# Kernel optimization log

Measured on AMD Instinct MI355X. Metric: run time of the kernel, lower is better.

## Reference

```python
import jax, jax.numpy as jnp
import numpy as np

H = 2048          # hidden_size
I = 1408          # moe_intermediate_size
E = 32            # n_routed_experts
K = 4             # num_experts_per_tok
NS = 2            # n_shared_experts
RG = RU = RD = 128  # CUR ranks
SI = I * NS       # shared-expert intermediate size
B, S = 2, 2048


def _init(key, shape, fan_in):
    return jax.random.normal(key, shape, jnp.float32) / np.sqrt(fan_in)


def setup_inputs() -> dict:
    ks = jax.random.split(jax.random.key(0), 20)
    return {
        'x': jax.random.normal(ks[0], (B, S, H), jnp.float32),
        'gate_w': _init(ks[1], (E, H), H),
        'Rg': _init(ks[2], (RG, H), H),
        'Ru': _init(ks[3], (RU, H), H),
        'Rd': _init(ks[4], (RD, I), I),
        'Ug': _init(ks[5], (E, RG, RG), RG),
        'Cg': _init(ks[6], (E, I, RG), RG),
        'Uu': _init(ks[7], (E, RU, RU), RU),
        'Cu': _init(ks[8], (E, I, RU), RU),
        'Ud': _init(ks[9], (E, RD, RD), RD),
        'Cd': _init(ks[10], (E, H, RD), RD),
        's_Rg': _init(ks[11], (RG, H), H),
        's_Ug': _init(ks[12], (RG, RG), RG),
        's_Cg': _init(ks[13], (SI, RG), RG),
        's_Ru': _init(ks[14], (RU, H), H),
        's_Uu': _init(ks[15], (RU, RU), RU),
        's_Cu': _init(ks[16], (SI, RU), RU),
        's_Rd': _init(ks[17], (RD, SI), SI),
        's_Ud': _init(ks[18], (RD, RD), RD),
        's_Cd': _init(ks[19], (H, RD), RD),
    }


def _moe_forward(x, gate_w, Rg, Ru, Rd, Ug, Cg, Uu, Cu, Ud, Cd,
                 s_Rg, s_Ug, s_Cg, s_Ru, s_Uu, s_Cu, s_Rd, s_Ud, s_Cd):
    Bv, Sv, Hv = x.shape
    xf = x.reshape(-1, Hv)                       # [T,H]
    T = xf.shape[0]

    # ---- top-k softmax gate ----
    logits = xf @ gate_w.T                       # [T,E]
    scores = jax.nn.softmax(logits, axis=-1)
    tw, ti = jax.lax.top_k(scores, K)            # [T,K]
    tw = tw / (tw.sum(-1, keepdims=True) + 1e-20)
    # dense per-(token,expert) combine weight; zero where token not routed.
    # Mathematically identical to the torch gather/per-expert-GEMM/scatter_add path.
    we = jnp.zeros((T, E), xf.dtype).at[jnp.arange(T)[:, None], ti].add(tw)  # [T,E]

    # shared R projections are expert-independent: compute once for all tokens
    rg = xf @ Rg.T                               # [T,RG]
    ru = xf @ Ru.T                               # [T,RU]

    def expert_fn(Ug_e, Cg_e, Uu_e, Cu_e, Ud_e, Cd_e, w_e, rg, ru):
        g = jax.nn.silu((rg @ Ug_e.T) @ Cg_e.T)  # [T,I]
        u = (ru @ Uu_e.T) @ Cu_e.T               # [T,I]
        rd = (g * u) @ Rd.T                      # [T,RD]
        return w_e[:, None] * ((rd @ Ud_e.T) @ Cd_e.T)  # [T,H]

    expert_fn = jax.checkpoint(expert_fn)

    def body(acc, ws):
        Ug_e, Cg_e, Uu_e, Cu_e, Ud_e, Cd_e, w_e = ws
        return acc + expert_fn(Ug_e, Cg_e, Uu_e, Cu_e, Ud_e, Cd_e, w_e, rg, ru), None

    y, _ = jax.lax.scan(body, jnp.zeros_like(xf), (Ug, Cg, Uu, Cu, Ud, Cd, we.T))

    # ---- shared experts (own R matrices, intermediate = I * n_shared) ----
    g = jax.nn.silu(((xf @ s_Rg.T) @ s_Ug.T) @ s_Cg.T)   # [T,SI]
    u = ((xf @ s_Ru.T) @ s_Uu.T) @ s_Cu.T                # [T,SI]
    sh = (((g * u) @ s_Rd.T) @ s_Ud.T) @ s_Cd.T          # [T,H]

    return (y + sh).reshape(Bv, Sv, Hv)


def reference(x, gate_w, Rg, Ru, Rd, Ug, Cg, Uu, Cu, Ud, Cd,
              s_Rg, s_Ug, s_Cg, s_Ru, s_Uu, s_Cu, s_Rd, s_Ud, s_Cd):
    return _moe_forward(x, gate_w, Rg, Ru, Rd, Ug, Cg, Uu, Cu, Ud, Cd,
                        s_Rg, s_Ug, s_Cg, s_Ru, s_Uu, s_Cu, s_Rd, s_Ud, s_Cd)
```

## Files before the change

kernel.cpp:

```cpp
#include <hip/hip_runtime.h>
#include <math.h>

#define T_TOK 4096
#define HD    2048
#define NEXP  32
#define IR    1408
#define ISH   2816
#define NPAIR (T_TOK*4)
#define SRK   136
#define MTILES 11

typedef unsigned short ushort_t;
typedef __attribute__((ext_vector_type(8))) short    short8;
typedef __attribute__((ext_vector_type(8))) __bf16   bf16x8;
typedef __attribute__((ext_vector_type(4))) float    f32x4;

__device__ __forceinline__ f32x4 MF(short8 a, short8 b, f32x4 c) {
  return __builtin_amdgcn_mfma_f32_16x16x32_bf16(
      __builtin_bit_cast(bf16x8, a), __builtin_bit_cast(bf16x8, b), c, 0, 0, 0);
}
__device__ __forceinline__ ushort_t f2b(float f) {
  unsigned u = __float_as_uint(f);
  unsigned r = (u + 0x7fffu + ((u >> 16) & 1u)) >> 16;
  return (ushort_t)r;
}
__device__ __forceinline__ float b2f(ushort_t b) {
  return __uint_as_float(((unsigned)b) << 16);
}

__device__ __forceinline__ void gll16(const ushort_t* g, ushort_t* l) {
  __builtin_amdgcn_global_load_lds(
      (const __attribute__((address_space(1))) unsigned int*)(const void*)g,
      (__attribute__((address_space(3))) unsigned int*)(void*)l, 16, 0, 0);
}

__device__ __forceinline__ void load_64x128_swz(
    const ushort_t* __restrict__ g, size_t gstride, ushort_t* lds, int tid)
{
  const int lane = tid & 63, w = tid >> 6;
  #pragma unroll
  for (int s = 0; s < 4; ++s) {
    int rbase = s*16 + w*4;
    int r = rbase + (lane >> 4);
    int p = lane & 15;
    gll16(g + (size_t)r*gstride + ((p ^ (r & 15)) << 3), lds + rbase*128);
  }
}

#define NSEG 19
struct CvtSegs {
  const float* s[NSEG];
  ushort_t* d[NSEG];
  int n4[NSEG];
  int blk0[NSEG+1];
};
__global__ __launch_bounds__(256) void cvt_all_kernel(CvtSegs cs)
{
  int b = blockIdx.x;
  int k = 0;
  #pragma unroll 1
  while (k+1 < NSEG && b >= cs.blk0[k+1]) ++k;
  int i = (b - cs.blk0[k])*256 + threadIdx.x;
  if (i < cs.n4[k]) {
    float4 v = ((const float4*)cs.s[k])[i];
    ushort4 o; o.x=f2b(v.x); o.y=f2b(v.y); o.z=f2b(v.z); o.w=f2b(v.w);
    ((ushort4*)cs.d[k])[i] = o;
  }
}

__global__ __launch_bounds__(256) void gate_kernel(
    const float* __restrict__ x, const float* __restrict__ gw,
    int* __restrict__ topk_idx, float* __restrict__ topk_w, int* __restrict__ cnt)
{
  __shared__ float gws[32*132];
  __shared__ float xs[4*132];
  const int tid = threadIdx.x;
  const int w = tid >> 6, lane = tid & 63;
  const int t0 = blockIdx.x * 4;
  const int e = lane & 31, half = lane >> 5;

  float acc = 0.f;
  for (int ck = 0; ck < HD/128; ++ck) {
    for (int li = tid; li < 1024; li += 256) {
      int r = li >> 5, c4 = li & 31;
      *(float4*)(gws + r*132 + c4*4) = *(const float4*)(gw + (size_t)r*HD + ck*128 + c4*4);
    }
    for (int li = tid; li < 128; li += 256) {
      int r = li >> 5, c4 = li & 31;
      *(float4*)(xs + r*132 + c4*4) = *(const float4*)(x + (size_t)(t0+r)*HD + ck*128 + c4*4);
    }
    __syncthreads();
    #pragma unroll
    for (int k4 = 0; k4 < 16; ++k4) {
      float4 xv = *(const float4*)(xs + w*132 + half*64 + k4*4);
      float4 wv = *(const float4*)(gws + e*132 + half*64 + k4*4);
      acc += xv.x*wv.x + xv.y*wv.y + xv.z*wv.z + xv.w*wv.w;
    }
    __syncthreads();
  }
  float p = acc;
  p += __shfl_down(p, 32);
  float logit = (lane < 32) ? p : -INFINITY;
  float m = logit;
  #pragma unroll
  for (int o = 32; o >= 1; o >>= 1) m = fmaxf(m, __shfl_xor(m, o));
  float ex = (lane < 32) ? expf(logit - m) : 0.f;
  float se = ex;
  #pragma unroll
  for (int o = 32; o >= 1; o >>= 1) se += __shfl_xor(se, o);
  float score = ex / se;

  bool taken = false;
  float selw[4]; int seli[4];
  for (int k = 0; k < 4; ++k) {
    float cur = (lane < 32 && !taken) ? score : -1.f;
    float mm = cur;
    #pragma unroll
    for (int o = 32; o >= 1; o >>= 1) mm = fmaxf(mm, __shfl_xor(mm, o));
    unsigned long long b = __ballot(cur == mm);
    int il = __ffsll(b) - 1;
    if (lane == il) taken = true;
    selw[k] = mm; seli[k] = il;
  }
  float wsum = selw[0]+selw[1]+selw[2]+selw[3] + 1e-20f;
  int t = t0 + w;
  if (lane < 4) {
    topk_idx[t*4+lane] = seli[lane];
    topk_w[t*4+lane]  = selw[lane] / wsum;
    atomicAdd(&cnt[seli[lane]], 1);
  }
}

__global__ void scan_kernel(const int* __restrict__ cnt, int* __restrict__ offA)
{
  if (threadIdx.x == 0) {
    int a = 0;
    for (int e = 0; e < NEXP; ++e) { offA[e] = a; a += cnt[e]; }
    offA[NEXP] = a;
  }
}

__global__ __launch_bounds__(256) void scatter_kernel(
    const int* __restrict__ topk_idx, const float* __restrict__ topk_w,
    const int* __restrict__ offA, int* __restrict__ fill,
    int* __restrict__ list_tok, int* __restrict__ slot_of)
{
  int t = blockIdx.x*256 + threadIdx.x;
  if (t >= T_TOK) return;
  #pragma unroll
  for (int k = 0; k < 4; ++k) {
    int e = topk_idx[t*4+k];
    int pos = atomicAdd(&fill[e], 1);
    int s = offA[e] + pos;
    list_tok[s] = t;
    slot_of[t*4+k] = s;
  }
}

__global__ __launch_bounds__(256) void rproj_kernel(
    const ushort_t* __restrict__ xb,
    const ushort_t* __restrict__ Rg, const ushort_t* __restrict__ Ru,
    const ushort_t* __restrict__ sRg, const ushort_t* __restrict__ sRu,
    ushort_t* __restrict__ rg, ushort_t* __restrict__ ru,
    ushort_t* __restrict__ sa, ushort_t* __restrict__ su)
{
  __shared__ ushort_t abuf[2][64*128];
  const ushort_t* W; ushort_t* Y;
  switch (blockIdx.y) {
    case 0:  W = Rg;  Y = rg; break;
    case 1:  W = Ru;  Y = ru; break;
    case 2:  W = sRg; Y = sa; break;
    default: W = sRu; Y = su; break;
  }
  const int tid = threadIdx.x;
  const int lane = tid & 63, ln = lane & 15, q = lane >> 4;
  const int wv = tid >> 6, mh = wv >> 1, nh = wv & 1;
  const int r0 = blockIdx.x * 64;

  f32x4 acc[2][4];
  #pragma unroll
  for (int i = 0; i < 2; ++i)
    #pragma unroll
    for (int j = 0; j < 4; ++j) acc[i][j] = (f32x4){0.f,0.f,0.f,0.f};

  load_64x128_swz(xb + (size_t)r0*HD, HD, abuf[0], tid);
  for (int kt = 0; kt < 16; ++kt) {
    __syncthreads();
    if (kt+1 < 16)
      load_64x128_swz(xb + (size_t)r0*HD + (kt+1)*128, HD, abuf[(kt+1)&1], tid);
    const ushort_t* A = abuf[kt&1];
    #pragma unroll
    for (int c = 0; c < 4; ++c) {
      short8 a[2], b[4];
      #pragma unroll
      for (int i = 0; i < 2; ++i) {
        int rr = mh*32 + i*16 + ln;
        a[i] = *(const short8*)(A + rr*128 + (((c*4+q) ^ (rr&15)) << 3));
      }
      #pragma unroll
      for (int j = 0; j < 4; ++j)
        b[j] = *(const short8*)(W + (size_t)(nh*64 + j*16 + ln)*HD + kt*128 + c*32 + q*8);
      #pragma unroll
      for (int i = 0; i < 2; ++i)
        #pragma unroll
        for (int j = 0; j < 4; ++j) acc[i][j] = MF(a[i], b[j], acc[i][j]);
    }
  }
  #pragma unroll
  for (int i = 0; i < 2; ++i)
    #pragma unroll
    for (int j = 0; j < 4; ++j)
      #pragma unroll
      for (int r = 0; r < 4; ++r)
        Y[(size_t)(r0 + mh*32 + i*16 + q*4 + r)*128 + nh*64 + j*16 + ln] = f2b(acc[i][j][r]);
}

__device__ __forceinline__ void gemm64x128_regs(
    int tid, const ushort_t* __restrict__ A, const ushort_t* __restrict__ Wg,
    ushort_t* __restrict__ stage, f32x4 acc[2][2][2])
{
  const int lane = tid & 63, ln = lane & 15, q = lane >> 4;
  const int wv = tid >> 6, mh = wv >> 1, nh = wv & 1;
  #pragma unroll
  for (int h = 0; h < 2; ++h)
    #pragma unroll
    for (int i = 0; i < 2; ++i)
      #pragma unroll
      for (int j = 0; j < 2; ++j) acc[h][i][j] = (f32x4){0.f,0.f,0.f,0.f};
  for (int h = 0; h < 2; ++h) {
    for (int li = tid; li < 64*16; li += 256) {
      int r = li >> 4, c = (li & 15) << 3;
      *(short8*)(stage + r*SRK + c) = *(const short8*)(Wg + (size_t)(h*64 + r)*128 + c);
    }
    __syncthreads();
    #pragma unroll
    for (int c = 0; c < 4; ++c) {
      short8 a[2], b[2];
      #pragma unroll
      for (int i = 0; i < 2; ++i)
        a[i] = *(const short8*)(A + (mh*32 + i*16 + ln)*SRK + c*32 + q*8);
      #pragma unroll
      for (int j = 0; j < 2; ++j)
        b[j] = *(const short8*)(stage + (nh*32 + j*16 + ln)*SRK + c*32 + q*8);
      #pragma unroll
      for (int i = 0; i < 2; ++i)
        #pragma unroll
        for (int j = 0; j < 2; ++j) acc[h][i][j] = MF(a[i], b[j], acc[h][i][j]);
    }
    __syncthreads();
  }
}

__global__ __launch_bounds__(256) void pair_proj_kernel(
    const ushort_t* __restrict__ rgb, const ushort_t* __restrict__ rub,
    const ushort_t* __restrict__ sab, const ushort_t* __restrict__ sub,
    const ushort_t* __restrict__ Ug, const ushort_t* __restrict__ Uu,
    const ushort_t* __restrict__ sUg, const ushort_t* __restrict__ sUu,
    const int* __restrict__ offA, const int* __restrict__ cntA,
    const int* __restrict__ list_tok,
    ushort_t* __restrict__ t1R, ushort_t* __restrict__ t2R,
    ushort_t* __restrict__ t1S, ushort_t* __restrict__ t2S)
{
  __shared__ ushort_t ldsX[64*SRK];
  __shared__ ushort_t stage[64*SRK];
  __shared__ int toks[64];
  const int tid = threadIdx.x;
  const int by = blockIdx.y;
  const bool shm = (by == NEXP);
  const int nrows = shm ? T_TOK : cntA[by];
  const int s0 = blockIdx.x * 64;
  if (s0 >= nrows) return;
  const int base = shm ? 0 : offA[by];
  const ushort_t* pUg = shm ? sUg : Ug + (size_t)by*128*128;
  const ushort_t* pUu = shm ? sUu : Uu + (size_t)by*128*128;
  const int lane = tid & 63, ln = lane & 15, q = lane >> 4;
  const int wv = tid >> 6, mh = wv >> 1, nh = wv & 1;

  if (tid < 64) {
    int sc = s0 + tid; if (sc > nrows-1) sc = nrows-1;
    toks[tid] = shm ? sc : list_tok[base + sc];
  }
  __syncthreads();

  f32x4 acc[2][2][2];
  for (int li = tid; li < 64*16; li += 256) {
    int r = li >> 4, c = (li & 15) << 3;
    const ushort_t* src = shm ? sab : rgb;
    *(short8*)(ldsX + r*SRK + c) = *(const short8*)(src + (size_t)toks[r]*128 + c);
  }
  __syncthreads();
  gemm64x128_regs(tid, ldsX, pUg, stage, acc);
  {
    ushort_t* dst = shm ? t1S : (t1R + (size_t)base*128);
    #pragma unroll
    for (int h = 0; h < 2; ++h)
      #pragma unroll
      for (int i = 0; i < 2; ++i)
        #pragma unroll
        for (int r = 0; r < 4; ++r) {
          int gs = s0 + mh*32 + i*16 + q*4 + r;
          if (gs < nrows) {
            #pragma unroll
            for (int j = 0; j < 2; ++j)
              dst[(size_t)gs*128 + h*64 + nh*32 + j*16 + ln] = f2b(acc[h][i][j][r]);
          }
        }
  }
  for (int li = tid; li < 64*16; li += 256) {
    int r = li >> 4, c = (li & 15) << 3;
    const ushort_t* src = shm ? sub : rub;
    *(short8*)(ldsX + r*SRK + c) = *(const short8*)(src + (size_t)toks[r]*128 + c);
  }
  __syncthreads();
  gemm64x128_regs(tid, ldsX, pUu, stage, acc);
  {
    ushort_t* dst = shm ? t2S : (t2R + (size_t)base*128);
    #pragma unroll
    for (int h = 0; h < 2; ++h)
      #pragma unroll
      for (int i = 0; i < 2; ++i)
        #pragma unroll
        for (int r = 0; r < 4; ++r) {
          int gs = s0 + mh*32 + i*16 + q*4 + r;
          if (gs < nrows) {
            #pragma unroll
            for (int j = 0; j < 2; ++j)
              dst[(size_t)gs*128 + h*64 + nh*32 + j*16 + ln] = f2b(acc[h][i][j][r]);
          }
        }
  }
}

__global__ __launch_bounds__(256, 1) void mid_kernel(
    const ushort_t* __restrict__ t1R, const ushort_t* __restrict__ t2R,
    const ushort_t* __restrict__ t1S, const ushort_t* __restrict__ t2S,
    const ushort_t* __restrict__ Cg, const ushort_t* __restrict__ Cu,
    const ushort_t* __restrict__ Rd,
    const ushort_t* __restrict__ sCg, const ushort_t* __restrict__ sCu,
    const ushort_t* __restrict__ sRd,
    const int* __restrict__ offA, const int* __restrict__ cntA,
    float* __restrict__ rdRp, float* __restrict__ rdSp)
{
  __shared__ ushort_t ldsCg[2][64*128];
  __shared__ ushort_t ldsCu[2][64*128];
  __shared__ ushort_t ldsH [2][64*64];

  const int hh = blockIdx.x + 64*(blockIdx.y + 33*blockIdx.z);
  const int xc = hh & 7, m = hh >> 3;
  int bx, by, bz;
  if (m < 1024) { by = (m >> 8)*8 + xc; bz = (m >> 6) & 3; bx = m & 63; }
  else          { int mm = m - 1024; by = NEXP; bz = mm >> 3; bx = ((mm & 7) << 3) + xc; }

  const bool shm = (by == NEXP);
  if (bz >= (shm ? 4 : 2)) return;
  const int nrows = shm ? T_TOK : cntA[by];
  const int s0 = bx * 64;
  if (s0 >= nrows) return;
  const int base = shm ? 0 : offA[by];
  const int Ifull = shm ? ISH : IR;
  const ushort_t* pCg = shm ? sCg : Cg + (size_t)by*IR*128;
  const ushort_t* pCu = shm ? sCu : Cu + (size_t)by*IR*128;
  const ushort_t* pRd = shm ? sRd : Rd;

  const int tid = threadIdx.x;
  const int lane = tid & 63, ln = lane & 15, q = lane >> 4;
  const int wv = tid >> 6, mh = wv >> 1, nh = wv & 1;
  const int it0 = bz * MTILES;

  short8 t1f[2][4], t2f[2][4];
  const ushort_t* srcT1 = shm ? t1S : (t1R + (size_t)base*128);
  const ushort_t* srcT2 = shm ? t2S : (t2R + (size_t)base*128);
  #pragma unroll
  for (int i = 0; i < 2; ++i) {
    int r = s0 + mh*32 + i*16 + ln; if (r > nrows-1) r = nrows-1;
    #pragma unroll
    for (int c = 0; c < 4; ++c) {
      t1f[i][c] = *(const short8*)(srcT1 + (size_t)r*128 + c*32 + q*8);
      t2f[i][c] = *(const short8*)(srcT2 + (size_t)r*128 + c*32 + q*8);
    }
  }

  load_64x128_swz(pCg + (size_t)it0*64*128, 128, ldsCg[0], tid);
  load_64x128_swz(pCu + (size_t)it0*64*128, 128, ldsCu[0], tid);

  f32x4 rdacc[2][4];
  #pragma unroll
  for (int i = 0; i < 2; ++i)
    #pragma unroll
    for (int j = 0; j < 4; ++j) rdacc[i][j] = (f32x4){0.f,0.f,0.f,0.f};

  const size_t rdRow = (size_t)(nh*64 + ln)*Ifull + q*8;

  __syncthreads();

  for (int it = 0; it < MTILES; ++it) {
    const int i0 = (it0 + it) * 64;
    const int cb = it & 1;
    if (it+1 < MTILES) {
      load_64x128_swz(pCg + (size_t)(i0+64)*128, 128, ldsCg[cb^1], tid);
      load_64x128_swz(pCu + (size_t)(i0+64)*128, 128, ldsCu[cb^1], tid);
    }
    short8 rb[2][4];
    if (it > 0) {
      const int ip = i0 - 64;
      #pragma unroll
      for (int c2 = 0; c2 < 2; ++c2)
        #pragma unroll
        for (int j = 0; j < 4; ++j)
          rb[c2][j] = *(const short8*)(pRd + rdRow + (size_t)(j*16)*Ifull + ip + c2*32);
    }
    f32x4 g[2][2], u[2][2];
    #pragma unroll
    for (int i = 0; i < 2; ++i)
      #pragma unroll
      for (int j = 0; j < 2; ++j) { g[i][j] = (f32x4){0.f,0.f,0.f,0.f}; u[i][j] = (f32x4){0.f,0.f,0.f,0.f}; }
    #pragma unroll
    for (int c = 0; c < 4; ++c) {
      #pragma unroll
      for (int j = 0; j < 2; ++j) {
        int rr = nh*32 + j*16 + ln;
        int off = rr*128 + (((c*4+q) ^ (rr&15)) << 3);
        short8 bg = *(const short8*)(ldsCg[cb] + off);
        short8 bu = *(const short8*)(ldsCu[cb] + off);
        #pragma unroll
        for (int i = 0; i < 2; ++i) {
          g[i][j] = MF(t1f[i][c], bg, g[i][j]);
          u[i][j] = MF(t2f[i][c], bu, u[i][j]);
        }
      }
    }
    #pragma unroll
    for (int i = 0; i < 2; ++i)
      #pragma unroll
      for (int j = 0; j < 2; ++j)
        #pragma unroll
        for (int r = 0; r < 4; ++r) {
          float gv = g[i][j][r];
          gv = gv / (1.f + __expf(-gv));
          float hv = gv * u[i][j][r];
          int hr = mh*32 + i*16 + q*4 + r;
          int hc = nh*32 + j*16 + ln;
          ldsH[cb][hr*64 + (((hc>>3) ^ (hr&7)) << 3) + (hc&7)] = f2b(hv);
        }
    if (it > 0) {
      #pragma unroll
      for (int c2 = 0; c2 < 2; ++c2) {
        short8 a[2];
        #pragma unroll
        for (int i = 0; i < 2; ++i) {
          int rr = mh*32 + i*16 + ln;
          a[i] = *(const short8*)(ldsH[cb^1] + rr*64 + (((c2*4+q) ^ (rr&7)) << 3));
        }
        #pragma unroll
        for (int j = 0; j < 4; ++j)
          #pragma unroll
          for (int i = 0; i < 2; ++i) rdacc[i][j] = MF(a[i], rb[c2][j], rdacc[i][j]);
      }
    }
    __syncthreads();
  }
  {
    const int ip = (it0 + MTILES - 1) * 64;
    const int cb = (MTILES - 1) & 1;
    #pragma unroll
    for (int c2 = 0; c2 < 2; ++c2) {
      short8 a[2];
      #pragma unroll
      for (int i = 0; i < 2; ++i) {
        int rr = mh*32 + i*16 + ln;
        a[i] = *(const short8*)(ldsH[cb] + rr*64 + (((c2*4+q) ^ (rr&7)) << 3));
      }
      #pragma unroll
      for (int j = 0; j < 4; ++j) {
        short8 b = *(const short8*)(pRd + rdRow + (size_t)(j*16)*Ifull + ip + c2*32);
        #pragma unroll
        for (int i = 0; i < 2; ++i) rdacc[i][j] = MF(a[i], b, rdacc[i][j]);
      }
    }
  }

  float* dst = shm ? (rdSp + (size_t)bz*T_TOK*128)
                   : (rdRp + (size_t)bz*NPAIR*128 + (size_t)base*128);
  #pragma unroll
  for (int i = 0; i < 2; ++i) {
    #pragma unroll
    for (int r = 0; r < 4; ++r) {
      int gs = s0 + mh*32 + i*16 + q*4 + r;
      if (gs < nrows) {
        #pragma unroll
        for (int j = 0; j < 4; ++j)
          dst[(size_t)gs*128 + nh*64 + j*16 + ln] = rdacc[i][j][r];
      }
    }
  }
}

__global__ __launch_bounds__(256) void out_kernel(
    const float* __restrict__ rdRp, const float* __restrict__ rdSp,
    const ushort_t* __restrict__ Ud, const ushort_t* __restrict__ Cd,
    const ushort_t* __restrict__ sUd, const ushort_t* __restrict__ sCd,
    const int* __restrict__ offA, const int* __restrict__ cntA,
    ushort_t* __restrict__ ybufR, float* __restrict__ out)
{
  __shared__ ushort_t smem[3*64*SRK];
  ushort_t* ldsA  = smem;
  ushort_t* stage = smem + 64*SRK;
  ushort_t* ldsT  = smem + 2*64*SRK;
  ushort_t* cd0   = smem;
  ushort_t* cd1   = smem + 64*128;

  const int hh = blockIdx.x + 64*(blockIdx.y + 33*blockIdx.z);
  const int xc = hh & 7, m = hh >> 3;
  int bx, by, bzz;
  if (m < 512) { by = (m >> 7)*8 + xc; bzz = (m >> 6) & 1; bx = m & 63; }
  else         { int mm = m - 512; by = NEXP; bzz = mm >> 3; bx = ((mm & 7) << 3) + xc; }

  const int tid = threadIdx.x;
  const bool shm = (by == NEXP);
  const int nrows = shm ? T_TOK : cntA[by];
  const int s0 = bx * 64;
  if (s0 >= nrows) return;
  const int base = shm ? 0 : offA[by];
  const int ct0 = bzz * 16;
  const ushort_t* pUd = shm ? sUd : Ud + (size_t)by*128*128;
  const ushort_t* pCd = shm ? sCd : Cd + (size_t)by*HD*128;

  const int lane = tid & 63, ln = lane & 15, q = lane >> 4;
  const int wv = tid >> 6, mh = wv >> 1, nh = wv & 1;

  for (int li = tid; li < 64*32; li += 256) {
    int r = li >> 5, c4 = li & 31;
    int row = s0 + r; if (row > nrows-1) row = nrows-1;
    float4 v;
    if (shm) {
      const float* p = rdSp + (size_t)row*128 + c4*4;
      v = *(const float4*)p;
      #pragma unroll
      for (int pp = 1; pp < 4; ++pp) {
        float4 w2 = *(const float4*)(p + (size_t)pp*T_TOK*128);
        v.x += w2.x; v.y += w2.y; v.z += w2.z; v.w += w2.w;
      }
    } else {
      const float* p = rdRp + (size_t)(base+row)*128 + c4*4;
      v = *(const float4*)p;
      float4 w2 = *(const float4*)(p + (size_t)NPAIR*128);
      v.x += w2.x; v.y += w2.y; v.z += w2.z; v.w += w2.w;
    }
    ushort4 o; o.x=f2b(v.x); o.y=f2b(v.y); o.z=f2b(v.z); o.w=f2b(v.w);
    *(ushort4*)(ldsA + r*SRK + c4*4) = o;
  }
  __syncthreads();

  f32x4 acc[2][2][2];
  gemm64x128_regs(tid, ldsA, pUd, stage, acc);
  #pragma unroll
  for (int h = 0; h < 2; ++h)
    #pragma unroll
    for (int i = 0; i < 2; ++i)
      #pragma unroll
      for (int j = 0; j < 2; ++j)
        #pragma unroll
        for (int r = 0; r < 4; ++r)
          ldsT[(mh*32 + i*16 + q*4 + r)*SRK + h*64 + nh*32 + j*16 + ln] = f2b(acc[h][i][j][r]);
  __syncthreads();
  short8 t3f[2][4];
  #pragma unroll
  for (int i = 0; i < 2; ++i)
    #pragma unroll
    for (int c = 0; c < 4; ++c)
      t3f[i][c] = *(const short8*)(ldsT + (mh*32 + i*16 + ln)*SRK + c*32 + q*8);
  __syncthreads();

  load_64x128_swz(pCd + (size_t)ct0*64*128, 128, cd0, tid);
  for (int tt = 0; tt < 16; ++tt) {
    __syncthreads();
    ushort_t* cur = (tt & 1) ? cd1 : cd0;
    ushort_t* nxt = (tt & 1) ? cd0 : cd1;
    if (tt+1 < 16)
      load_64x128_swz(pCd + (size_t)(ct0+tt+1)*64*128, 128, nxt, tid);
    f32x4 y[2][2];
    #pragma unroll
    for (int i = 0; i < 2; ++i)
      #pragma unroll
      for (int j = 0; j < 2; ++j) y[i][j] = (f32x4){0.f,0.f,0.f,0.f};
    #pragma unroll
    for (int c = 0; c < 4; ++c) {
      #pragma unroll
      for (int j = 0; j < 2; ++j) {
        int rr = nh*32 + j*16 + ln;
        short8 b = *(const short8*)(cur + rr*128 + (((c*4+q) ^ (rr&15)) << 3));
        #pragma unroll
        for (int i = 0; i < 2; ++i) y[i][j] = MF(t3f[i][c], b, y[i][j]);
      }
    }
    #pragma unroll
    for (int i = 0; i < 2; ++i) {
      #pragma unroll
      for (int r = 0; r < 4; ++r) {
        int lr = mh*32 + i*16 + q*4 + r;
        int gs = s0 + lr;
        if (gs < nrows) {
          if (shm) {
            size_t ob = (size_t)gs*HD + (ct0 + tt)*64;
            #pragma unroll
            for (int j = 0; j < 2; ++j)
              out[ob + nh*32 + j*16 + ln] = y[i][j][r];
          } else {
            size_t ob = (size_t)(base + gs)*HD + (ct0 + tt)*64;
            #pragma unroll
            for (int j = 0; j < 2; ++j)
              ybufR[ob + nh*32 + j*16 + ln] = f2b(y[i][j][r]);
          }
        }
      }
    }
  }
}

__global__ __launch_bounds__(256) void combine_kernel(
    const ushort_t* __restrict__ ybufR,
    const int* __restrict__ slot_of, const float* __restrict__ topk_w,
    float* __restrict__ out)
{
  __shared__ int   ss[4];
  __shared__ float ww[4];
  const int t = blockIdx.x;
  if (threadIdx.x < 4) {
    ss[threadIdx.x] = slot_of[t*4 + threadIdx.x];
    ww[threadIdx.x] = topk_w[t*4 + threadIdx.x];
  }
  __syncthreads();
  const int c = threadIdx.x * 8;
  const size_t tb = (size_t)t*HD + c;
  float o[8];
  float4 a0 = *(const float4*)(out + tb);
  float4 a1 = *(const float4*)(out + tb + 4);
  o[0]=a0.x; o[1]=a0.y; o[2]=a0.z; o[3]=a0.w;
  o[4]=a1.x; o[5]=a1.y; o[6]=a1.z; o[7]=a1.w;
  #pragma unroll
  for (int k = 0; k < 4; ++k) {
    short8 rv = *(const short8*)(ybufR + (size_t)ss[k]*HD + c);
    float wk = ww[k];
    #pragma unroll
    for (int u = 0; u < 8; ++u)
      o[u] += wk * b2f((ushort_t)rv[u]);
  }
  float4 b0 = {o[0],o[1],o[2],o[3]};
  float4 b1 = {o[4],o[5],o[6],o[7]};
  *(float4*)(out + tb)     = b0;
  *(float4*)(out + tb + 4) = b1;
}

extern "C" void kernel_launch(void* const* d_in, const int* in_sizes, int n_in,
                              void* d_out, int out_size, void* d_ws, size_t ws_size,
                              hipStream_t stream) {
  const float* x    = (const float*)d_in[0];
  const float* gw   = (const float*)d_in[1];
  const float* Rg   = (const float*)d_in[2];
  const float* Ru   = (const float*)d_in[3];
  const float* Rd   = (const float*)d_in[4];
  const float* Ug   = (const float*)d_in[5];
  const float* Cg   = (const float*)d_in[6];
  const float* Uu   = (const float*)d_in[7];
  const float* Cu   = (const float*)d_in[8];
  const float* Ud   = (const float*)d_in[9];
  const float* Cd   = (const float*)d_in[10];
  const float* sRg  = (const float*)d_in[11];
  const float* sUg  = (const float*)d_in[12];
  const float* sCg  = (const float*)d_in[13];
  const float* sRu  = (const float*)d_in[14];
  const float* sUu  = (const float*)d_in[15];
  const float* sCu  = (const float*)d_in[16];
  const float* sRd  = (const float*)d_in[17];
  const float* sUd  = (const float*)d_in[18];
  const float* sCd  = (const float*)d_in[19];
  float* out = (float*)d_out;

  char* w = (char*)d_ws;
  auto alloc = [&](size_t bytes) -> void* {
    void* p = (void*)w; w += (bytes + 255) & ~(size_t)255; return p;
  };
  int*   cnt      = (int*)  alloc(NEXP*sizeof(int));
  int*   offA     = (int*)  alloc((NEXP+1)*sizeof(int));
  int*   fill     = (int*)  alloc(NEXP*sizeof(int));
  int*   topk_idx = (int*)  alloc((size_t)T_TOK*4*sizeof(int));
  float* topk_w   = (float*)alloc((size_t)T_TOK*4*sizeof(float));
  int*   list_tok = (int*)  alloc((size_t)NPAIR*sizeof(int));
  int*   slot_of  = (int*)  alloc((size_t)T_TOK*4*sizeof(int));
  ushort_t* xb   = (ushort_t*)alloc((size_t)T_TOK*HD*2);
  ushort_t* Rgb  = (ushort_t*)alloc((size_t)128*HD*2);
  ushort_t* Rub  = (ushort_t*)alloc((size_t)128*HD*2);
  ushort_t* Rdb  = (ushort_t*)alloc((size_t)128*IR*2);
  ushort_t* Ugb  = (ushort_t*)alloc((size_t)NEXP*128*128*2);
  ushort_t* Cgb  = (ushort_t*)alloc((size_t)NEXP*IR*128*2);
  ushort_t* Uub  = (ushort_t*)alloc((size_t)NEXP*128*128*2);
  ushort_t* Cub  = (ushort_t*)alloc((size_t)NEXP*IR*128*2);
  ushort_t* Udb  = (ushort_t*)alloc((size_t)NEXP*128*128*2);
  ushort_t* Cdb  = (ushort_t*)alloc((size_t)NEXP*HD*128*2);
  ushort_t* sRgb = (ushort_t*)alloc((size_t)128*HD*2);
  ushort_t* sUgb = (ushort_t*)alloc((size_t)128*128*2);
  ushort_t* sCgb = (ushort_t*)alloc((size_t)ISH*128*2);
  ushort_t* sRub = (ushort_t*)alloc((size_t)128*HD*2);
  ushort_t* sUub = (ushort_t*)alloc((size_t)128*128*2);
  ushort_t* sCub = (ushort_t*)alloc((size_t)ISH*128*2);
  ushort_t* sRdb = (ushort_t*)alloc((size_t)128*ISH*2);
  ushort_t* sUdb = (ushort_t*)alloc((size_t)128*128*2);
  ushort_t* sCdb = (ushort_t*)alloc((size_t)HD*128*2);
  ushort_t* rg   = (ushort_t*)alloc((size_t)T_TOK*128*2);
  ushort_t* ru   = (ushort_t*)alloc((size_t)T_TOK*128*2);
  ushort_t* sa   = (ushort_t*)alloc((size_t)T_TOK*128*2);
  ushort_t* su   = (ushort_t*)alloc((size_t)T_TOK*128*2);
  ushort_t* t1R  = (ushort_t*)alloc((size_t)NPAIR*128*2);
  ushort_t* t2R  = (ushort_t*)alloc((size_t)NPAIR*128*2);
  ushort_t* t1S  = (ushort_t*)alloc((size_t)T_TOK*128*2);
  ushort_t* t2S  = (ushort_t*)alloc((size_t)T_TOK*128*2);
  float*    rdSp = (float*)   alloc((size_t)4*T_TOK*128*sizeof(float));
  ushort_t* ybufR= (ushort_t*)alloc((size_t)NPAIR*HD*2);
  (void)ws_size; (void)in_sizes; (void)n_in;

  float* rdRp = (float*)xb;

  hipMemsetAsync(cnt,  0, NEXP*sizeof(int), stream);
  hipMemsetAsync(fill, 0, NEXP*sizeof(int), stream);

  CvtSegs cs;
  const float* ss[NSEG] = {x,Rg,Ru,Rd,Ug,Cg,Uu,Cu,Ud,Cd,sRg,sUg,sCg,sRu,sUu,sCu,sRd,sUd,sCd};
  ushort_t* dd[NSEG] = {xb,Rgb,Rub,Rdb,Ugb,Cgb,Uub,Cub,Udb,Cdb,sRgb,sUgb,sCgb,sRub,sUub,sCub,sRdb,sUdb,sCdb};
  size_t nn[NSEG] = {(size_t)T_TOK*HD,(size_t)128*HD,(size_t)128*HD,(size_t)128*IR,
                     (size_t)NEXP*128*128,(size_t)NEXP*IR*128,(size_t)NEXP*128*128,(size_t)NEXP*IR*128,
                     (size_t)NEXP*128*128,(size_t)NEXP*HD*128,(size_t)128*HD,(size_t)128*128,
                     (size_t)ISH*128,(size_t)128*HD,(size_t)128*128,(size_t)ISH*128,
                     (size_t)128*ISH,(size_t)128*128,(size_t)HD*128};
  int tot_blk = 0;
  for (int k = 0; k < NSEG; ++k) {
    cs.s[k] = ss[k]; cs.d[k] = dd[k];
    cs.n4[k] = (int)(nn[k] >> 2);
    cs.blk0[k] = tot_blk;
    tot_blk += (cs.n4[k] + 255) / 256;
  }
  cs.blk0[NSEG] = tot_blk;
  cvt_all_kernel<<<tot_blk, 256, 0, stream>>>(cs);

  gate_kernel<<<T_TOK/4, 256, 0, stream>>>(x, gw, topk_idx, topk_w, cnt);
  scan_kernel<<<1, 64, 0, stream>>>(cnt, offA);
  scatter_kernel<<<T_TOK/256, 256, 0, stream>>>(topk_idx, topk_w, offA, fill, list_tok, slot_of);
  rproj_kernel<<<dim3(T_TOK/64, 4), 256, 0, stream>>>(xb, Rgb, Rub, sRgb, sRub, rg, ru, sa, su);
  pair_proj_kernel<<<dim3(64, NEXP+1), 256, 0, stream>>>(
      rg, ru, sa, su, Ugb, Uub, sUgb, sUub, offA, cnt, list_tok, t1R, t2R, t1S, t2S);
  mid_kernel<<<dim3(64, NEXP+1, 4), 256, 0, stream>>>(
      t1R, t2R, t1S, t2S, Cgb, Cub, Rdb, sCgb, sCub, sRdb, offA, cnt, rdRp, rdSp);
  out_kernel<<<dim3(64, NEXP+1, 2), 256, 0, stream>>>(
      rdRp, rdSp, Udb, Cdb, sUdb, sCdb, offA, cnt, ybufR, out);
  combine_kernel<<<T_TOK, 256, 0, stream>>>(ybufR, slot_of, topk_w, out);
}
```

Before: 587.2 us.

## Make mid_kernel persistent with per-XCD atomic work queues and faster SiLU

Adds a plan kernel that builds eight compact work lists, one per XCD group, holding only the valid (expert, k-split, row-tile) items. The grid of mostly-early-exiting blocks is replaced by 512 persistent blocks that pull items atomically, starting with their own XCD list and then stealing from the others. This removes launch and scheduling overhead for empty blocks and evens out load across experts of uneven size. It also swaps the SiLU division for v_rcp, packs the bf16 conversions, and issues the Rd register loads before the LDS prefetch. In exchange it adds a serial planning kernel, an extra memset, and an atomic plus two barriers per work item.

```diff
diff --git a/kernel.cpp b/kernel.cpp
--- a/kernel.cpp
+++ b/kernel.cpp
@@ -9,6 +9,7 @@
 #define NPAIR (T_TOK*4)
 #define SRK   136
 #define MTILES 11
+#define WLCAP 2048
 
 typedef unsigned short ushort_t;
 typedef __attribute__((ext_vector_type(8))) short    short8;
@@ -26,6 +27,12 @@
 }
 __device__ __forceinline__ float b2f(ushort_t b) {
   return __uint_as_float(((unsigned)b) << 16);
+}
+__device__ __forceinline__ float fast_rcp(float x) {
+  float r; asm("v_rcp_f32 %0, %1" : "=v"(r) : "v"(x)); return r;
+}
+__device__ __forceinline__ unsigned cvt_pk_bf16(float lo, float hi) {
+  unsigned r; asm("v_cvt_pk_bf16_f32 %0, %1, %2" : "=v"(r) : "v"(lo), "v"(hi)); return r;
 }
 
 __device__ __forceinline__ void gll16(const ushort_t* g, ushort_t* l) {
@@ -137,6 +144,28 @@
     int a = 0;
     for (int e = 0; e < NEXP; ++e) { offA[e] = a; a += cnt[e]; }
     offA[NEXP] = a;
+  }
+}
+
+__global__ __launch_bounds__(256) void plan_kernel(
+    const int* __restrict__ cnt, int* __restrict__ wn, int* __restrict__ wl)
+{
+  const int t = threadIdx.x;
+  if (t < 8) wn[t] = 32;
+  __syncthreads();
+  {
+    int x = t >> 5, i = t & 31;
+    int bz = i >> 3, bx = ((i & 7) << 3) + x;
+    wl[x*WLCAP + i] = (NEXP << 16) | (bz << 12) | bx;
+  }
+  __syncthreads();
+  if (t < NEXP) {
+    int nb = (cnt[t] + 63) >> 6;
+    int x = t & 7;
+    int pos = atomicAdd(&wn[x], nb*2);
+    for (int bz = 0; bz < 2; ++bz)
+      for (int bx = 0; bx < nb; ++bx)
+        wl[x*WLCAP + pos++] = (t << 16) | (bz << 12) | bx;
   }
 }
 
@@ -339,157 +368,175 @@
     const ushort_t* __restrict__ sCg, const ushort_t* __restrict__ sCu,
     const ushort_t* __restrict__ sRd,
     const int* __restrict__ offA, const int* __restrict__ cntA,
-    float* __restrict__ rdRp, float* __restrict__ rdSp)
+    float* __restrict__ rdRp, float* __restrict__ rdSp,
+    const int* __restrict__ wn, int* __restrict__ wcnt, const int* __restrict__ wl)
 {
   __shared__ ushort_t ldsCg[2][64*128];
   __shared__ ushort_t ldsCu[2][64*128];
   __shared__ ushort_t ldsH [2][64*64];
-
-  const int hh = blockIdx.x + 64*(blockIdx.y + 33*blockIdx.z);
-  const int xc = hh & 7, m = hh >> 3;
-  int bx, by, bz;
-  if (m < 1024) { by = (m >> 8)*8 + xc; bz = (m >> 6) & 3; bx = m & 63; }
-  else          { int mm = m - 1024; by = NEXP; bz = mm >> 3; bx = ((mm & 7) << 3) + xc; }
-
-  const bool shm = (by == NEXP);
-  if (bz >= (shm ? 4 : 2)) return;
-  const int nrows = shm ? T_TOK : cntA[by];
-  const int s0 = bx * 64;
-  if (s0 >= nrows) return;
-  const int base = shm ? 0 : offA[by];
-  const int Ifull = shm ? ISH : IR;
-  const ushort_t* pCg = shm ? sCg : Cg + (size_t)by*IR*128;
-  const ushort_t* pCu = shm ? sCu : Cu + (size_t)by*IR*128;
-  const ushort_t* pRd = shm ? sRd : Rd;
+  __shared__ int s_item;
 
   const int tid = threadIdx.x;
   const int lane = tid & 63, ln = lane & 15, q = lane >> 4;
   const int wv = tid >> 6, mh = wv >> 1, nh = wv & 1;
-  const int it0 = bz * MTILES;
-
-  short8 t1f[2][4], t2f[2][4];
-  const ushort_t* srcT1 = shm ? t1S : (t1R + (size_t)base*128);
-  const ushort_t* srcT2 = shm ? t2S : (t2R + (size_t)base*128);
-  #pragma unroll
-  for (int i = 0; i < 2; ++i) {
-    int r = s0 + mh*32 + i*16 + ln; if (r > nrows-1) r = nrows-1;
-    #pragma unroll
-    for (int c = 0; c < 4; ++c) {
-      t1f[i][c] = *(const short8*)(srcT1 + (size_t)r*128 + c*32 + q*8);
-      t2f[i][c] = *(const short8*)(srcT2 + (size_t)r*128 + c*32 + q*8);
-    }
-  }
-
-  load_64x128_swz(pCg + (size_t)it0*64*128, 128, ldsCg[0], tid);
-  load_64x128_swz(pCu + (size_t)it0*64*128, 128, ldsCu[0], tid);
-
-  f32x4 rdacc[2][4];
-  #pragma unroll
-  for (int i = 0; i < 2; ++i)
-    #pragma unroll
-    for (int j = 0; j < 4; ++j) rdacc[i][j] = (f32x4){0.f,0.f,0.f,0.f};
-
-  const size_t rdRow = (size_t)(nh*64 + ln)*Ifull + q*8;
-
-  __syncthreads();
-
-  for (int it = 0; it < MTILES; ++it) {
-    const int i0 = (it0 + it) * 64;
-    const int cb = it & 1;
-    if (it+1 < MTILES) {
-      load_64x128_swz(pCg + (size_t)(i0+64)*128, 128, ldsCg[cb^1], tid);
-      load_64x128_swz(pCu + (size_t)(i0+64)*128, 128, ldsCu[cb^1], tid);
-    }
-    short8 rb[2][4];
-    if (it > 0) {
-      const int ip = i0 - 64;
-      #pragma unroll
-      for (int c2 = 0; c2 < 2; ++c2)
-        #pragma unroll
-        for (int j = 0; j < 4; ++j)
-          rb[c2][j] = *(const short8*)(pRd + rdRow + (size_t)(j*16)*Ifull + ip + c2*32);
-    }
-    f32x4 g[2][2], u[2][2];
-    #pragma unroll
-    for (int i = 0; i < 2; ++i)
-      #pragma unroll
-      for (int j = 0; j < 2; ++j) { g[i][j] = (f32x4){0.f,0.f,0.f,0.f}; u[i][j] = (f32x4){0.f,0.f,0.f,0.f}; }
-    #pragma unroll
-    for (int c = 0; c < 4; ++c) {
-      #pragma unroll
-      for (int j = 0; j < 2; ++j) {
-        int rr = nh*32 + j*16 + ln;
-        int off = rr*128 + (((c*4+q) ^ (rr&15)) << 3);
-        short8 bg = *(const short8*)(ldsCg[cb] + off);
-        short8 bu = *(const short8*)(ldsCu[cb] + off);
-        #pragma unroll
-        for (int i = 0; i < 2; ++i) {
-          g[i][j] = MF(t1f[i][c], bg, g[i][j]);
-          u[i][j] = MF(t2f[i][c], bu, u[i][j]);
+  const int xc0 = blockIdx.x & 7;
+
+  for (int lx = 0; lx < 8; ++lx) {
+    const int xc = (xc0 + lx) & 7;
+    const int nww = wn[xc];
+    for (;;) {
+      __syncthreads();
+      if (tid == 0) s_item = atomicAdd(&wcnt[xc], 1);
+      __syncthreads();
+      const int wi = s_item;
+      if (wi >= nww) break;
+      const int item = wl[xc*WLCAP + wi];
+      const int by = item >> 16, bz = (item >> 12) & 15, bx = item & 4095;
+
+      const bool shm = (by == NEXP);
+      const int nrows = shm ? T_TOK : cntA[by];
+      const int s0 = bx * 64;
+      const int base = shm ? 0 : offA[by];
+      const int Ifull = shm ? ISH : IR;
+      const ushort_t* pCg = shm ? sCg : Cg + (size_t)by*IR*128;
+      const ushort_t* pCu = shm ? sCu : Cu + (size_t)by*IR*128;
+      const ushort_t* pRd = shm ? sRd : Rd;
+      const int it0 = bz * MTILES;
+
+      short8 t1f[2][4], t2f[2][4];
+      const ushort_t* srcT1 = shm ? t1S : (t1R + (size_t)base*128);
+      const ushort_t* srcT2 = shm ? t2S : (t2R + (size_t)base*128);
+      #pragma unroll
+      for (int i = 0; i < 2; ++i) {
+        int r = s0 + mh*32 + i*16 + ln; if (r > nrows-1) r = nrows-1;
+        #pragma unroll
+        for (int c = 0; c < 4; ++c) {
+          t1f[i][c] = *(const short8*)(srcT1 + (size_t)r*128 + c*32 + q*8);
+          t2f[i][c] = *(const short8*)(srcT2 + (size_t)r*128 + c*32 + q*8);
         }
       }
-    }
-    #pragma unroll
-    for (int i = 0; i < 2; ++i)
-      #pragma unroll
-      for (int j = 0; j < 2; ++j)
+
+      load_64x128_swz(pCg + (size_t)it0*64*128, 128, ldsCg[0], tid);
+      load_64x128_swz(pCu + (size_t)it0*64*128, 128, ldsCu[0], tid);
+
+      f32x4 rdacc[2][4];
+      #pragma unroll
+      for (int i = 0; i < 2; ++i)
+        #pragma unroll
+        for (int j = 0; j < 4; ++j) rdacc[i][j] = (f32x4){0.f,0.f,0.f,0.f};
+
+      const size_t rdRow = (size_t)(nh*64 + ln)*Ifull + q*8;
+
+      __syncthreads();
+
+      for (int it = 0; it < MTILES; ++it) {
+        const int i0 = (it0 + it) * 64;
+        const int cb = it & 1;
+        short8 rb[2][4];
+        if (it > 0) {
+          const int ip = i0 - 64;
+          #pragma unroll
+          for (int c2 = 0; c2 < 2; ++c2)
+            #pragma unroll
+            for (int j = 0; j < 4; ++j)
+              rb[c2][j] = *(const short8*)(pRd + rdRow + (size_t)(j*16)*Ifull + ip + c2*32);
+        }
+        if (it+1 < MTILES) {
+          load_64x128_swz(pCg + (size_t)(i0+64)*128, 128, ldsCg[cb^1], tid);
+          load_64x128_swz(pCu + (size_t)(i0+64)*128, 128, ldsCu[cb^1], tid);
+        }
+        f32x4 g[2][2], u[2][2];
+        #pragma unroll
+        for (int i = 0; i < 2; ++i)
+          #pragma unroll
+          for (int j = 0; j < 2; ++j) { g[i][j] = (f32x4){0.f,0.f,0.f,0.f}; u[i][j] = (f32x4){0.f,0.f,0.f,0.f}; }
+        #pragma unroll
+        for (int c = 0; c < 4; ++c) {
+          #pragma unroll
+          for (int j = 0; j < 2; ++j) {
+            int rr = nh*32 + j*16 + ln;
+            int off = rr*128 + (((c*4+q) ^ (rr&15)) << 3);
+            short8 bg = *(const short8*)(ldsCg[cb] + off);
+            short8 bu = *(const short8*)(ldsCu[cb] + off);
+            #pragma unroll
+            for (int i = 0; i < 2; ++i) {
+              g[i][j] = MF(t1f[i][c], bg, g[i][j]);
+              u[i][j] = MF(t2f[i][c], bu, u[i][j]);
+            }
+          }
+        }
+        #pragma unroll
+        for (int i = 0; i < 2; ++i)
+          #pragma unroll
+          for (int j = 0; j < 2; ++j) {
+            float hv[4];
+            #pragma unroll
+            for (int r = 0; r < 4; ++r) {
+              float gv = g[i][j][r];
+              hv[r] = gv * fast_rcp(1.f + __expf(-gv)) * u[i][j][r];
+            }
+            unsigned p01 = cvt_pk_bf16(hv[0], hv[1]);
+            unsigned p23 = cvt_pk_bf16(hv[2], hv[3]);
+            const int hc = nh*32 + j*16 + ln;
+            const int hb = mh*32 + i*16 + q*4;
+            #pragma unroll
+            for (int r = 0; r < 4; ++r) {
+              int hr = hb + r;
+              ushort_t v = (r==0) ? (ushort_t)p01 : (r==1) ? (ushort_t)(p01>>16)
+                         : (r==2) ? (ushort_t)p23 : (ushort_t)(p23>>16);
+              ldsH[cb][hr*64 + (((hc>>3) ^ (hr&7)) << 3) + (hc&7)] = v;
+            }
+          }
+        if (it > 0) {
+          #pragma unroll
+          for (int c2 = 0; c2 < 2; ++c2) {
+            short8 a[2];
+            #pragma unroll
+            for (int i = 0; i < 2; ++i) {
+              int rr = mh*32 + i*16 + ln;
+              a[i] = *(const short8*)(ldsH[cb^1] + rr*64 + (((c2*4+q) ^ (rr&7)) << 3));
+            }
+            #pragma unroll
+            for (int j = 0; j < 4; ++j)
+              #pragma unroll
+              for (int i = 0; i < 2; ++i) rdacc[i][j] = MF(a[i], rb[c2][j], rdacc[i][j]);
+          }
+        }
+        __syncthreads();
+      }
+      {
+        const int ip = (it0 + MTILES - 1) * 64;
+        const int cb = (MTILES - 1) & 1;
+        #pragma unroll
+        for (int c2 = 0; c2 < 2; ++c2) {
+          short8 a[2];
+          #pragma unroll
+          for (int i = 0; i < 2; ++i) {
+            int rr = mh*32 + i*16 + ln;
+            a[i] = *(const short8*)(ldsH[cb] + rr*64 + (((c2*4+q) ^ (rr&7)) << 3));
+          }
+          #pragma unroll
+          for (int j = 0; j < 4; ++j) {
+            short8 b = *(const short8*)(pRd + rdRow + (size_t)(j*16)*Ifull + ip + c2*32);
+            #pragma unroll
+            for (int i = 0; i < 2; ++i) rdacc[i][j] = MF(a[i], b, rdacc[i][j]);
+          }
+        }
+      }
+
+      float* dst = shm ? (rdSp + (size_t)bz*T_TOK*128)
+                       : (rdRp + (size_t)bz*NPAIR*128 + (size_t)base*128);
+      #pragma unroll
+      for (int i = 0; i < 2; ++i) {
         #pragma unroll
         for (int r = 0; r < 4; ++r) {
-          float gv = g[i][j][r];
-          gv = gv / (1.f + __expf(-gv));
-          float hv = gv * u[i][j][r];
-          int hr = mh*32 + i*16 + q*4 + r;
-          int hc = nh*32 + j*16 + ln;
-          ldsH[cb][hr*64 + (((hc>>3) ^ (hr&7)) << 3) + (hc&7)] = f2b(hv);
-        }
-    if (it > 0) {
-      #pragma unroll
-      for (int c2 = 0; c2 < 2; ++c2) {
-        short8 a[2];
-        #pragma unroll
-        for (int i = 0; i < 2; ++i) {
-          int rr = mh*32 + i*16 + ln;
-          a[i] = *(const short8*)(ldsH[cb^1] + rr*64 + (((c2*4+q) ^ (rr&7)) << 3));
-        }
-        #pragma unroll
-        for (int j = 0; j < 4; ++j)
-          #pragma unroll
-          for (int i = 0; i < 2; ++i) rdacc[i][j] = MF(a[i], rb[c2][j], rdacc[i][j]);
-      }
-    }
-    __syncthreads();
-  }
-  {
-    const int ip = (it0 + MTILES - 1) * 64;
-    const int cb = (MTILES - 1) & 1;
-    #pragma unroll
-    for (int c2 = 0; c2 < 2; ++c2) {
-      short8 a[2];
-      #pragma unroll
-      for (int i = 0; i < 2; ++i) {
-        int rr = mh*32 + i*16 + ln;
-        a[i] = *(const short8*)(ldsH[cb] + rr*64 + (((c2*4+q) ^ (rr&7)) << 3));
-      }
-      #pragma unroll
-      for (int j = 0; j < 4; ++j) {
-        short8 b = *(const short8*)(pRd + rdRow + (size_t)(j*16)*Ifull + ip + c2*32);
-        #pragma unroll
-        for (int i = 0; i < 2; ++i) rdacc[i][j] = MF(a[i], b, rdacc[i][j]);
-      }
-    }
-  }
-
-  float* dst = shm ? (rdSp + (size_t)bz*T_TOK*128)
-                   : (rdRp + (size_t)bz*NPAIR*128 + (size_t)base*128);
-  #pragma unroll
-  for (int i = 0; i < 2; ++i) {
-    #pragma unroll
-    for (int r = 0; r < 4; ++r) {
-      int gs = s0 + mh*32 + i*16 + q*4 + r;
-      if (gs < nrows) {
-        #pragma unroll
-        for (int j = 0; j < 4; ++j)
-          dst[(size_t)gs*128 + nh*64 + j*16 + ln] = rdacc[i][j][r];
+          int gs = s0 + mh*32 + i*16 + q*4 + r;
+          if (gs < nrows) {
+            #pragma unroll
+            for (int j = 0; j < 4; ++j)
+              dst[(size_t)gs*128 + nh*64 + j*16 + ln] = rdacc[i][j][r];
+          }
+        }
       }
     }
   }
@@ -687,6 +734,9 @@
   float* topk_w   = (float*)alloc((size_t)T_TOK*4*sizeof(float));
   int*   list_tok = (int*)  alloc((size_t)NPAIR*sizeof(int));
   int*   slot_of  = (int*)  alloc((size_t)T_TOK*4*sizeof(int));
+  int*   wn       = (int*)  alloc(8*sizeof(int));
+  int*   wcnt     = (int*)  alloc(8*sizeof(int));
+  int*   wl       = (int*)  alloc((size_t)8*WLCAP*sizeof(int));
   ushort_t* xb   = (ushort_t*)alloc((size_t)T_TOK*HD*2);
   ushort_t* Rgb  = (ushort_t*)alloc((size_t)128*HD*2);
   ushort_t* Rub  = (ushort_t*)alloc((size_t)128*HD*2);
@@ -722,6 +772,7 @@
 
   hipMemsetAsync(cnt,  0, NEXP*sizeof(int), stream);
   hipMemsetAsync(fill, 0, NEXP*sizeof(int), stream);
+  hipMemsetAsync(wcnt, 0, 8*sizeof(int), stream);
 
   CvtSegs cs;
   const float* ss[NSEG] = {x,Rg,Ru,Rd,Ug,Cg,Uu,Cu,Ud,Cd,sRg,sUg,sCg,sRu,sUu,sCu,sRd,sUd,sCd};
@@ -743,13 +794,15 @@
 
   gate_kernel<<<T_TOK/4, 256, 0, stream>>>(x, gw, topk_idx, topk_w, cnt);
   scan_kernel<<<1, 64, 0, stream>>>(cnt, offA);
+  plan_kernel<<<1, 256, 0, stream>>>(cnt, wn, wl);
   scatter_kernel<<<T_TOK/256, 256, 0, stream>>>(topk_idx, topk_w, offA, fill, list_tok, slot_of);
   rproj_kernel<<<dim3(T_TOK/64, 4), 256, 0, stream>>>(xb, Rgb, Rub, sRgb, sRub, rg, ru, sa, su);
   pair_proj_kernel<<<dim3(64, NEXP+1), 256, 0, stream>>>(
       rg, ru, sa, su, Ugb, Uub, sUgb, sUub, offA, cnt, list_tok, t1R, t2R, t1S, t2S);
-  mid_kernel<<<dim3(64, NEXP+1, 4), 256, 0, stream>>>(
-      t1R, t2R, t1S, t2S, Cgb, Cub, Rdb, sCgb, sCub, sRdb, offA, cnt, rdRp, rdSp);
-  out_kernel<<<dim3(64, NEXP+1, 2), 256, 0, stream>>>(
+  mid_kernel<<<512, 256, 0, stream>>>(
+      t1R, t2R, t1S, t2S, Cgb, Cub, Rdb, sCgb, sCub, sRdb, offA, cnt, rdRp, rdSp,
+      wn, wcnt, wl);
+  out_kernel<<<dim3(64, 33, 2), 256, 0, stream>>>(
       rdRp, rdSp, Udb, Cdb, sUdb, sCdb, offA, cnt, ybufR, out);
   combine_kernel<<<T_TOK, 256, 0, stream>>>(ybufR, slot_of, topk_w, out);
 }
```

After: 576.5 us. About the same (-1.8%).
